# Kernel tuning notes

Measured on AMD Instinct MI355X. Metric: run time of the kernel, lower is better.

The kernel has to match this reference:

```python
import jax, jax.numpy as jnp
import numpy as np

B, T, C = 4, 2048, 1024
H, D = 16, 64


def setup_inputs() -> dict:
    key = jax.random.key(0)
    ks = jax.random.split(key, 5)
    x = jax.random.normal(ks[0], (B, T, C), dtype=jnp.float32)
    Wq = jax.random.normal(ks[1], (H, C, D), dtype=jnp.float32) * (C ** -0.5)
    Wk = jax.random.normal(ks[2], (H, C, D), dtype=jnp.float32) * (C ** -0.5)
    Wv = jax.random.normal(ks[3], (H, C, D), dtype=jnp.float32) * (C ** -0.5)
    Wp = jax.random.normal(ks[4], (H * D, C), dtype=jnp.float32) * ((H * D) ** -0.5)
    bp = jnp.zeros((C,), dtype=jnp.float32)
    return {"x": x, "Wq": Wq, "Wk": Wk, "Wv": Wv, "Wp": Wp, "bp": bp}


def reference(x, Wq, Wk, Wv, Wp, bp):
    # per-head projections (bias-free): [B,H,T,D]
    q = jnp.einsum('btc,hcd->bhtd', x, Wq)
    k = jnp.einsum('btc,hcd->bhtd', x, Wk)
    v = jnp.einsum('btc,hcd->bhtd', x, Wv)
    # NOTE: source multiplies by sqrt(head_size) (faithful to original code)
    scale = jnp.asarray(D ** 0.5, x.dtype)
    att = jnp.einsum('bhtd,bhsd->bhts', q, k) * scale  # [B,H,T,T]
    causal = jnp.tril(jnp.ones((T, T), dtype=bool))
    att = jnp.where(causal, att, jnp.asarray(-jnp.inf, att.dtype))
    att = jax.nn.softmax(att, axis=-1)
    out = jnp.einsum('bhts,bhsd->bhtd', att, v)  # [B,H,T,D]
    out = out.transpose(0, 2, 1, 3).reshape(B, T, H * D)  # head concat
    return out @ Wp + bp
```

## Files before the change

kernel.cpp:

```cpp
#include <hip/hip_runtime.h>

#define B_ 4
#define T_ 2048
#define C_ 1024
#define H_ 16
#define D_ 64

typedef _Float16 f16x8 __attribute__((ext_vector_type(8)));
typedef __fp16 fp16x2 __attribute__((ext_vector_type(2)));
typedef float f32x4 __attribute__((ext_vector_type(4)));
typedef unsigned short u16x8 __attribute__((ext_vector_type(8)));

#define MFMA16 __builtin_amdgcn_mfma_f32_16x16x32_f16
#define SCALE2 11.541560327111707f

__device__ __forceinline__ unsigned pk2(float a, float b) {
    fp16x2 p = __builtin_amdgcn_cvt_pkrtz(a, b);
    return __builtin_bit_cast(unsigned, p);
}

__device__ __forceinline__ void gl_lds16(const _Float16* g, unsigned short* lds) {
    __builtin_amdgcn_global_load_lds(
        (const __attribute__((address_space(1))) unsigned int*)g,
        (__attribute__((address_space(3))) unsigned int*)lds, 16, 0, 0);
}

__global__ __launch_bounds__(256) void convx_kernel(const float* __restrict__ x,
                                                    _Float16* __restrict__ Xf) {
    size_t i = ((size_t)blockIdx.x * 256 + threadIdx.x) * 8;
    f32x4 a = *reinterpret_cast<const f32x4*>(x + i);
    f32x4 b = *reinterpret_cast<const f32x4*>(x + i + 4);
    f16x8 o;
    o[0] = (_Float16)a[0]; o[1] = (_Float16)a[1]; o[2] = (_Float16)a[2]; o[3] = (_Float16)a[3];
    o[4] = (_Float16)b[0]; o[5] = (_Float16)b[1]; o[6] = (_Float16)b[2]; o[7] = (_Float16)b[3];
    *reinterpret_cast<f16x8*>(Xf + i) = o;
}

__global__ __launch_bounds__(256) void convw_qkv_kernel(
    const float* __restrict__ Wq, const float* __restrict__ Wk, const float* __restrict__ Wv,
    _Float16* __restrict__ Wqt, _Float16* __restrict__ Wkt, _Float16* __restrict__ Wvt)
{
    __shared__ unsigned short Wl[128][72];
    const int ct = blockIdx.x, h = blockIdx.y, m = blockIdx.z;
    const float* src = (m == 0 ? Wq : (m == 1 ? Wk : Wv)) + ((size_t)h * C_ + ct * 128) * D_;
    _Float16* dst = (m == 0 ? Wqt : (m == 1 ? Wkt : Wvt));
    const int tid = threadIdx.x;
    {
        int r = tid >> 1, half = tid & 1;
        #pragma unroll
        for (int i = 0; i < 8; i++) {
            f32x4 v = *reinterpret_cast<const f32x4*>(src + (size_t)r * D_ + half * 32 + i * 4);
            #pragma unroll
            for (int j = 0; j < 4; j++)
                Wl[r][half * 32 + i * 4 + j] = __builtin_bit_cast(unsigned short, (_Float16)v[j]);
        }
    }
    __syncthreads();
    {
        int d = tid >> 2, seg = tid & 3;
        #pragma unroll
        for (int i = 0; i < 4; i++) {
            u16x8 o;
            #pragma unroll
            for (int j = 0; j < 8; j++) o[j] = Wl[seg * 32 + i * 8 + j][d];
            *reinterpret_cast<u16x8*>((unsigned short*)dst + ((size_t)h * D_ + d) * C_ + ct * 128 + seg * 32 + i * 8) = o;
        }
    }
}

__global__ __launch_bounds__(256) void convw_p_kernel(const float* __restrict__ Wp,
                                                      _Float16* __restrict__ Wpt)
{
    __shared__ unsigned short Pl[64][72];
    const int jt = blockIdx.x, kt = blockIdx.y;
    const int tid = threadIdx.x;
    {
        int r = tid >> 2, seg = tid & 3;
        #pragma unroll
        for (int i = 0; i < 4; i++) {
            f32x4 v = *reinterpret_cast<const f32x4*>(Wp + (size_t)(kt * 64 + r) * C_ + jt * 64 + seg * 16 + i * 4);
            #pragma unroll
            for (int j = 0; j < 4; j++)
                Pl[r][seg * 16 + i * 4 + j] = __builtin_bit_cast(unsigned short, (_Float16)v[j]);
        }
    }
    __syncthreads();
    {
        int jj = tid >> 2, kseg = tid & 3;
        #pragma unroll
        for (int i = 0; i < 2; i++) {
            u16x8 o;
            #pragma unroll
            for (int j = 0; j < 8; j++) o[j] = Pl[kseg * 16 + i * 8 + j][jj];
            *reinterpret_cast<u16x8*>((unsigned short*)Wpt + (size_t)(jt * 64 + jj) * C_ + kt * 64 + kseg * 16 + i * 8) = o;
        }
    }
}

__global__ __launch_bounds__(256) void qkv4_kernel(
    const _Float16* __restrict__ Xf, const _Float16* __restrict__ Wcat,
    _Float16* __restrict__ Qf, _Float16* __restrict__ Kf, _Float16* __restrict__ Vt)
{
    __shared__ unsigned short As[128 * 64];
    __shared__ unsigned short Bs[192 * 64];
    const int rt = blockIdx.x, ct = blockIdx.y;
    const int row0 = rt * 128, n0 = ct * 192;
    const int tid = threadIdx.x, wid = tid >> 6, lane = tid & 63;
    const int l15 = lane & 15, g = lane >> 4;
    const int wr = wid >> 1, wc = wid & 1;
    const int lrow = lane >> 3, lcol = (lane & 7) * 8;

    f32x4 acc[4][6];
    #pragma unroll
    for (int mi = 0; mi < 4; mi++)
        #pragma unroll
        for (int ni = 0; ni < 6; ni++) { f32x4 z = {0.f,0.f,0.f,0.f}; acc[mi][ni] = z; }

    for (int k0 = 0; k0 < C_; k0 += 64) {
        __syncthreads();
        #pragma unroll
        for (int i = 0; i < 4; i++) {
            int c = wid * 4 + i;
            gl_lds16(Xf + (size_t)(row0 + c * 8 + lrow) * C_ + k0 + lcol, &As[c * 512]);
        }
        #pragma unroll
        for (int i = 0; i < 6; i++) {
            int c = wid * 6 + i;
            gl_lds16(Wcat + (size_t)(n0 + c * 8 + lrow) * C_ + k0 + lcol, &Bs[c * 512]);
        }
        __syncthreads();
        #pragma unroll
        for (int kk = 0; kk < 2; kk++) {
            f16x8 af[4];
            #pragma unroll
            for (int mi = 0; mi < 4; mi++)
                af[mi] = *reinterpret_cast<const f16x8*>(&As[(wr * 64 + mi * 16 + l15) * 64 + kk * 32 + g * 8]);
            #pragma unroll
            for (int ni = 0; ni < 6; ni++) {
                f16x8 bf = *reinterpret_cast<const f16x8*>(&Bs[(wc * 96 + ni * 16 + l15) * 64 + kk * 32 + g * 8]);
                #pragma unroll
                for (int mi = 0; mi < 4; mi++)
                    acc[mi][ni] = MFMA16(af[mi], bf, acc[mi][ni], 0, 0, 0);
            }
        }
    }

    const int b = row0 >> 11;
    const int t0b = (row0 & (T_ - 1)) + wr * 64;
    #pragma unroll
    for (int ni = 0; ni < 6; ni++) {
        const int n = n0 + wc * 96 + ni * 16;
        const int region = n >> 10;
        const int h = (n >> 6) & 15;
        const int d0 = n & 63;
        if (region < 2) {
            _Float16* dst = region ? Kf : Qf;
            const float osc = region ? 1.0f : SCALE2;
            const size_t hb = ((size_t)(b * H_ + h)) * T_ * D_;
            #pragma unroll
            for (int mi = 0; mi < 4; mi++)
                #pragma unroll
                for (int r = 0; r < 4; r++) {
                    int t = t0b + mi * 16 + g * 4 + r;
                    dst[hb + (size_t)t * D_ + d0 + l15] = (_Float16)(acc[mi][ni][r] * osc);
                }
        } else {
            const size_t vbase = ((size_t)(b * H_ + h)) * D_ * T_;
            const int d = d0 + l15;
            #pragma unroll
            for (int mi = 0; mi < 4; mi++) {
                int t = t0b + mi * 16 + g * 4;
                uint2 w;
                w.x = pk2(acc[mi][ni][0], acc[mi][ni][1]);
                w.y = pk2(acc[mi][ni][2], acc[mi][ni][3]);
                *reinterpret_cast<uint2*>((unsigned short*)Vt + vbase + (size_t)d * T_ + t) = w;
            }
        }
    }
}

__global__ __launch_bounds__(256) void flash_kernel(
    const _Float16* __restrict__ Qf, const _Float16* __restrict__ Kf,
    const _Float16* __restrict__ Vt, _Float16* __restrict__ att)
{
    __shared__ __align__(16) unsigned short Ks[2][64 * 64];
    __shared__ __align__(16) unsigned short Vs[2][64 * 64];
    __shared__ __align__(16) unsigned short Ps[4][32 * 32];
    const int bh = blockIdx.x;
    const int p = (int)blockIdx.y;
    const int bb = bh >> 4, h = bh & 15;
    const int tid = threadIdx.x, wid = tid >> 6, lane = tid & 63;
    const int l15 = lane & 15, g = lane >> 4;

    const _Float16* Qb = Qf + (size_t)bh * T_ * D_;
    const _Float16* Kb = Kf + (size_t)bh * T_ * D_;
    const _Float16* Vb = Vt + (size_t)bh * D_ * T_;

    const int srow = lane >> 3;
    const int sunit = (lane & 7) ^ srow;
    const int r0s = wid * 16;

    char* const pbase = (char*)&Ps[wid][0];

    for (int pass = 0; pass < 2; pass++) {
        const int qt = pass ? p : (15 - p);
        const int q0 = qt * 128;
        const int qw = q0 + wid * 32;

        f16x8 qf[2][2];
        #pragma unroll
        for (int mt = 0; mt < 2; mt++)
            #pragma unroll
            for (int kk = 0; kk < 2; kk++)
                qf[mt][kk] = *reinterpret_cast<const f16x8*>(Qb + (size_t)(qw + mt * 16 + l15) * D_ + kk * 32 + g * 8);

        f32x4 accO[4][2];
        #pragma unroll
        for (int nt = 0; nt < 4; nt++)
            #pragma unroll
            for (int mt = 0; mt < 2; mt++) { f32x4 z = {0.f,0.f,0.f,0.f}; accO[nt][mt] = z; }
        float m[2] = { -1e30f, -1e30f };
        float l[2] = { 0.f, 0.f };

        const int myNt = (qw + 95) >> 6;
        const int ntB  = (q0 + 191) >> 6;

        #pragma unroll
        for (int i = 0; i < 2; i++) {
            int row = r0s + i * 8 + srow;
            gl_lds16(Kb + (size_t)row * D_ + sunit * 8, &Ks[0][(r0s + i * 8) * 64]);
            gl_lds16(Vb + (size_t)row * T_ + sunit * 8, &Vs[0][(r0s + i * 8) * 64]);
        }
        __syncthreads();

#define TILE_BODY(TI, BUF)                                                          \
    {                                                                               \
        const int kv0 = (TI) * 64;                                                  \
        if ((TI) + 1 < ntB) {                                                       \
            const int kvn = kv0 + 64;                                               \
            _Pragma("unroll")                                                       \
            for (int i = 0; i < 2; i++) {                                           \
                int row = r0s + i * 8 + srow;                                       \
                gl_lds16(Kb + (size_t)(kvn + row) * D_ + sunit * 8,                 \
                         &Ks[(BUF) ^ 1][(r0s + i * 8) * 64]);                       \
                gl_lds16(Vb + (size_t)row * T_ + kvn + sunit * 8,                   \
                         &Vs[(BUF) ^ 1][(r0s + i * 8) * 64]);                       \
            }                                                                       \
        }                                                                           \
        if ((TI) < myNt) {                                                          \
            const bool maskt = ((TI) == myNt - 1);                                  \
            const char* kbase = (const char*)&Ks[BUF][0];                           \
            const char* vbase = (const char*)&Vs[BUF][0];                           \
            f32x4 s[4][2];                                                          \
            _Pragma("unroll")                                                       \
            for (int st = 0; st < 4; st++)                                          \
                _Pragma("unroll")                                                   \
                for (int mt = 0; mt < 2; mt++) { f32x4 z = {0.f,0.f,0.f,0.f}; s[st][mt] = z; } \
            _Pragma("unroll")                                                       \
            for (int kk = 0; kk < 2; kk++) {                                        \
                f16x8 kfr[4];                                                       \
                _Pragma("unroll")                                                   \
                for (int st = 0; st < 4; st++) {                                    \
                    int row = st * 16 + l15;                                        \
                    kfr[st] = *reinterpret_cast<const f16x8*>(                      \
                        kbase + row * 128 + (((kk * 4 + g) ^ (row & 7)) * 16));     \
                }                                                                   \
                _Pragma("unroll")                                                   \
                for (int st = 0; st < 4; st++)                                      \
                    _Pragma("unroll")                                               \
                    for (int mt = 0; mt < 2; mt++)                                  \
                        s[st][mt] = MFMA16(kfr[st], qf[mt][kk], s[st][mt], 0, 0, 0);\
            }                                                                       \
            unsigned pw[2][4][2];                                                   \
            _Pragma("unroll")                                                       \
            for (int mt = 0; mt < 2; mt++) {                                        \
                const int r = mt * 16 + l15;                                        \
                const int qrow = qw + r;                                            \
                float lv[4][4];                                                     \
                float vmax = -1e30f;                                                \
                _Pragma("unroll")                                                   \
                for (int st = 0; st < 4; st++)                                      \
                    _Pragma("unroll")                                               \
                    for (int rr = 0; rr < 4; rr++) {                                \
                        float v = s[st][mt][rr];                                    \
                        if (maskt) {                                                \
                            int kv = kv0 + st * 16 + g * 4 + rr;                    \
                            v = (kv <= qrow) ? v : -1e30f;                          \
                        }                                                           \
                        lv[st][rr] = v;                                             \
                        vmax = fmaxf(vmax, v);                                      \
                    }                                                               \
                vmax = fmaxf(vmax, __shfl_xor(vmax, 16, 64));                       \
                vmax = fmaxf(vmax, __shfl_xor(vmax, 32, 64));                       \
                float mnew = fmaxf(m[mt], vmax);                                    \
                float alpha = __builtin_amdgcn_exp2f(m[mt] - mnew);                 \
                m[mt] = mnew;                                                       \
                float rs = 0.f;                                                     \
                _Pragma("unroll")                                                   \
                for (int st = 0; st < 4; st++) {                                    \
                    float p0 = __builtin_amdgcn_exp2f(lv[st][0] - mnew);            \
                    float p1 = __builtin_amdgcn_exp2f(lv[st][1] - mnew);            \
                    float p2 = __builtin_amdgcn_exp2f(lv[st][2] - mnew);            \
                    float p3 = __builtin_amdgcn_exp2f(lv[st][3] - mnew);            \
                    rs += (p0 + p1) + (p2 + p3);                                    \
                    pw[mt][st][0] = pk2(p0, p1);                                    \
                    pw[mt][st][1] = pk2(p2, p3);                                    \
                }                                                                   \
                rs += __shfl_xor(rs, 16, 64);                                       \
                rs += __shfl_xor(rs, 32, 64);                                       \
                l[mt] = l[mt] * alpha + rs;                                         \
                _Pragma("unroll")                                                   \
                for (int nt = 0; nt < 4; nt++) accO[nt][mt] *= alpha;               \
            }                                                                       \
            _Pragma("unroll")                                                       \
            for (int half = 0; half < 2; half++) {                                  \
                _Pragma("unroll")                                                   \
                for (int mt = 0; mt < 2; mt++) {                                    \
                    const int r = mt * 16 + l15;                                    \
                    const int swz = ((r >> 1) & 3) << 4;                            \
                    char* prow = pbase + r * 64;                                    \
                    _Pragma("unroll")                                               \
                    for (int stl = 0; stl < 2; stl++) {                             \
                        uint2 w;                                                    \
                        w.x = pw[mt][half * 2 + stl][0];                            \
                        w.y = pw[mt][half * 2 + stl][1];                            \
                        *reinterpret_cast<uint2*>(prow + ((stl * 32 + g * 8) ^ swz)) = w; \
                    }                                                               \
                }                                                                   \
                f16x8 pb[2];                                                        \
                _Pragma("unroll")                                                   \
                for (int mt = 0; mt < 2; mt++) {                                    \
                    const int r = mt * 16 + l15;                                    \
                    const int swz = ((r >> 1) & 3) << 4;                            \
                    pb[mt] = *reinterpret_cast<const f16x8*>(pbase + r * 64 + ((g * 16) ^ swz)); \
                }                                                                   \
                _Pragma("unroll")                                                   \
                for (int nt = 0; nt < 4; nt++) {                                    \
                    int row = nt * 16 + l15;                                        \
                    f16x8 vf = *reinterpret_cast<const f16x8*>(                     \
                        vbase + row * 128 + (((half * 4 + g) ^ (row & 7)) * 16));   \
                    _Pragma("unroll")                                               \
                    for (int mt = 0; mt < 2; mt++)                                  \
                        accO[nt][mt] = MFMA16(vf, pb[mt], accO[nt][mt], 0, 0, 0);   \
                }                                                                   \
            }                                                                       \
        }                                                                           \
        __syncthreads();                                                            \
    }

        for (int tI = 0; tI < ntB; tI += 2) {
            TILE_BODY(tI, 0)
            if (tI + 1 < ntB) {
                TILE_BODY(tI + 1, 1)
            }
        }
#undef TILE_BODY

        #pragma unroll
        for (int mt = 0; mt < 2; mt++) {
            float inv = 1.0f / l[mt];
            int t = qw + mt * 16 + l15;
            #pragma unroll
            for (int nt = 0; nt < 4; nt++) {
                f32x4 o = accO[nt][mt] * inv;
                uint2 w;
                w.x = pk2(o[0], o[1]);
                w.y = pk2(o[2], o[3]);
                size_t off = ((size_t)(bb * T_ + t)) * (H_ * D_) + h * D_ + nt * 16 + g * 4;
                *reinterpret_cast<uint2*>((unsigned short*)att + off) = w;
            }
        }
    }
}

__global__ __launch_bounds__(256) void proj2_kernel(
    const _Float16* __restrict__ att, const _Float16* __restrict__ Wpt,
    const float* __restrict__ bp, float* __restrict__ out)
{
    __shared__ unsigned short As[128 * 64];
    __shared__ unsigned short Bs[128 * 64];
    const int rt = blockIdx.x, ct = blockIdx.y;
    const int row0 = rt * 128, n0 = ct * 128;
    const int tid = threadIdx.x, wid = tid >> 6, lane = tid & 63;
    const int l15 = lane & 15, g = lane >> 4;
    const int wr = wid >> 1, wc = wid & 1;
    const int lrow = lane >> 3, lcol = (lane & 7) * 8;

    f32x4 acc[4][4];
    #pragma unroll
    for (int mi = 0; mi < 4; mi++)
        #pragma unroll
        for (int ni = 0; ni < 4; ni++) { f32x4 z = {0.f,0.f,0.f,0.f}; acc[mi][ni] = z; }

    for (int k0 = 0; k0 < C_; k0 += 64) {
        __syncthreads();
        #pragma unroll
        for (int i = 0; i < 4; i++) {
            int c = wid * 4 + i;
            gl_lds16(att + (size_t)(row0 + c * 8 + lrow) * C_ + k0 + lcol, &As[c * 512]);
            gl_lds16(Wpt + (size_t)(n0   + c * 8 + lrow) * C_ + k0 + lcol, &Bs[c * 512]);
        }
        __syncthreads();
        #pragma unroll
        for (int kk = 0; kk < 2; kk++) {
            f16x8 af[4], bf[4];
            #pragma unroll
            for (int mi = 0; mi < 4; mi++)
                af[mi] = *reinterpret_cast<const f16x8*>(&As[(wr * 64 + mi * 16 + l15) * 64 + kk * 32 + g * 8]);
            #pragma unroll
            for (int ni = 0; ni < 4; ni++)
                bf[ni] = *reinterpret_cast<const f16x8*>(&Bs[(wc * 64 + ni * 16 + l15) * 64 + kk * 32 + g * 8]);
            #pragma unroll
            for (int mi = 0; mi < 4; mi++)
                #pragma unroll
                for (int ni = 0; ni < 4; ni++)
                    acc[mi][ni] = MFMA16(af[mi], bf[ni], acc[mi][ni], 0, 0, 0);
        }
    }

    #pragma unroll
    for (int mi = 0; mi < 4; mi++)
        #pragma unroll
        for (int ni = 0; ni < 4; ni++) {
            int col = n0 + wc * 64 + ni * 16 + l15;
            float bias = bp[col];
            #pragma unroll
            for (int r = 0; r < 4; r++) {
                int row = row0 + wr * 64 + mi * 16 + g * 4 + r;
                out[(size_t)row * C_ + col] = acc[mi][ni][r] + bias;
            }
        }
}

extern "C" void kernel_launch(void* const* d_in, const int* in_sizes, int n_in,
                              void* d_out, int out_size, void* d_ws, size_t ws_size,
                              hipStream_t stream) {
    const float* x  = (const float*)d_in[0];
    const float* Wq = (const float*)d_in[1];
    const float* Wk = (const float*)d_in[2];
    const float* Wv = (const float*)d_in[3];
    const float* Wp = (const float*)d_in[4];
    const float* bp = (const float*)d_in[5];
    float* out = (float*)d_out;

    _Float16* Xf  = (_Float16*)d_ws;
    _Float16* Wqt = Xf  + (size_t)8388608;
    _Float16* Wkt = Wqt + (size_t)1048576;
    _Float16* Wvt = Wkt + (size_t)1048576;
    _Float16* Wpt = Wvt + (size_t)1048576;
    _Float16* Qf  = Wpt + (size_t)1048576;
    _Float16* Kf  = Qf  + (size_t)8388608;
    _Float16* Vt  = Kf  + (size_t)8388608;
    _Float16* att = Vt  + (size_t)8388608;

    convx_kernel<<<4096, 256, 0, stream>>>(x, Xf);
    convw_qkv_kernel<<<dim3(8, 16, 3), 256, 0, stream>>>(Wq, Wk, Wv, Wqt, Wkt, Wvt);
    convw_p_kernel<<<dim3(16, 16), 256, 0, stream>>>(Wp, Wpt);
    qkv4_kernel<<<dim3(64, 16), 256, 0, stream>>>(Xf, Wqt, Qf, Kf, Vt);
    flash_kernel<<<dim3(64, 8), 256, 0, stream>>>(Qf, Kf, Vt, att);
    proj2_kernel<<<dim3(64, 8), 256, 0, stream>>>(att, Wpt, bp, out);
}
```

Measured before the change: 195.5 us.

## Stage 128-row KV super-tiles in LDS and skip rescale when max unchanged

The flash attention kernel now loads K and V into LDS in 128-key super-tiles, double-buffered, and runs two 64-key sub-tiles per super-tile. This halves the number of block-wide barriers and prefetch rounds per query tile. It also adds a wave-uniform check that skips the accumulator and row-sum rescale when no row max increased. The cost is double the LDS footprint, which may reduce occupancy, and some extra masked work on the diagonal super-tile.

```diff
diff --git a/kernel.cpp b/kernel.cpp
--- a/kernel.cpp
+++ b/kernel.cpp
@@ -183,8 +183,8 @@
     const _Float16* __restrict__ Qf, const _Float16* __restrict__ Kf,
     const _Float16* __restrict__ Vt, _Float16* __restrict__ att)
 {
-    __shared__ __align__(16) unsigned short Ks[2][64 * 64];
-    __shared__ __align__(16) unsigned short Vs[2][64 * 64];
+    __shared__ __align__(16) unsigned short Ks[2][128 * 64];
+    __shared__ __align__(16) unsigned short Vs[2][64 * 128];
     __shared__ __align__(16) unsigned short Ps[4][32 * 32];
     const int bh = blockIdx.x;
     const int p = (int)blockIdx.y;
@@ -198,7 +198,9 @@
 
     const int srow = lane >> 3;
     const int sunit = (lane & 7) ^ srow;
-    const int r0s = wid * 16;
+    const int r0k = wid * 32;
+    const int vsrow = lane >> 4;
+    const int r0v = wid * 16;
 
     char* const pbase = (char*)&Ps[wid][0];
 
@@ -222,139 +224,150 @@
         float m[2] = { -1e30f, -1e30f };
         float l[2] = { 0.f, 0.f };
 
-        const int myNt = (qw + 95) >> 6;
-        const int ntB  = (q0 + 191) >> 6;
-
-        #pragma unroll
-        for (int i = 0; i < 2; i++) {
-            int row = r0s + i * 8 + srow;
-            gl_lds16(Kb + (size_t)row * D_ + sunit * 8, &Ks[0][(r0s + i * 8) * 64]);
-            gl_lds16(Vb + (size_t)row * T_ + sunit * 8, &Vs[0][(r0s + i * 8) * 64]);
+        const int nSup = qt + 1;
+        const int mySub = (qw + 95) >> 6;
+
+        #pragma unroll
+        for (int i = 0; i < 4; i++) {
+            int krow = r0k + i * 8 + srow;
+            gl_lds16(Kb + (size_t)krow * D_ + sunit * 8, &Ks[0][(r0k + i * 8) * 64]);
+            int vrow = r0v + i * 4 + vsrow;
+            int vsunit = (lane & 15) ^ (vrow & 7);
+            gl_lds16(Vb + (size_t)vrow * T_ + vsunit * 8, &Vs[0][(r0v + i * 4) * 128]);
         }
         __syncthreads();
 
-#define TILE_BODY(TI, BUF)                                                          \
+#define SUPER_BODY(SP, BUF)                                                         \
     {                                                                               \
-        const int kv0 = (TI) * 64;                                                  \
-        if ((TI) + 1 < ntB) {                                                       \
-            const int kvn = kv0 + 64;                                               \
+        if ((SP) + 1 < nSup) {                                                      \
+            const int kvn = ((SP) + 1) * 128;                                       \
             _Pragma("unroll")                                                       \
-            for (int i = 0; i < 2; i++) {                                           \
-                int row = r0s + i * 8 + srow;                                       \
-                gl_lds16(Kb + (size_t)(kvn + row) * D_ + sunit * 8,                 \
-                         &Ks[(BUF) ^ 1][(r0s + i * 8) * 64]);                       \
-                gl_lds16(Vb + (size_t)row * T_ + kvn + sunit * 8,                   \
-                         &Vs[(BUF) ^ 1][(r0s + i * 8) * 64]);                       \
+            for (int i = 0; i < 4; i++) {                                           \
+                int krow = r0k + i * 8 + srow;                                      \
+                gl_lds16(Kb + (size_t)(kvn + krow) * D_ + sunit * 8,                \
+                         &Ks[(BUF) ^ 1][(r0k + i * 8) * 64]);                       \
+                int vrow = r0v + i * 4 + vsrow;                                     \
+                int vsunit = (lane & 15) ^ (vrow & 7);                              \
+                gl_lds16(Vb + (size_t)vrow * T_ + kvn + vsunit * 8,                 \
+                         &Vs[(BUF) ^ 1][(r0v + i * 4) * 128]);                      \
             }                                                                       \
         }                                                                           \
-        if ((TI) < myNt) {                                                          \
-            const bool maskt = ((TI) == myNt - 1);                                  \
-            const char* kbase = (const char*)&Ks[BUF][0];                           \
-            const char* vbase = (const char*)&Vs[BUF][0];                           \
-            f32x4 s[4][2];                                                          \
-            _Pragma("unroll")                                                       \
-            for (int st = 0; st < 4; st++)                                          \
+        const char* kb128 = (const char*)&Ks[BUF][0];                               \
+        const char* vb128 = (const char*)&Vs[BUF][0];                               \
+        _Pragma("unroll")                                                           \
+        for (int sh = 0; sh < 2; sh++) {                                            \
+            const int sI = (SP) * 2 + sh;                                           \
+            if (sI < mySub) {                                                       \
+                const int kv0 = sI * 64;                                            \
+                const bool maskt = (sI == mySub - 1);                               \
+                f32x4 s[4][2];                                                      \
                 _Pragma("unroll")                                                   \
-                for (int mt = 0; mt < 2; mt++) { f32x4 z = {0.f,0.f,0.f,0.f}; s[st][mt] = z; } \
-            _Pragma("unroll")                                                       \
-            for (int kk = 0; kk < 2; kk++) {                                        \
-                f16x8 kfr[4];                                                       \
+                for (int st = 0; st < 4; st++)                                      \
+                    _Pragma("unroll")                                               \
+                    for (int mt = 0; mt < 2; mt++) { f32x4 z = {0.f,0.f,0.f,0.f}; s[st][mt] = z; } \
                 _Pragma("unroll")                                                   \
-                for (int st = 0; st < 4; st++) {                                    \
-                    int row = st * 16 + l15;                                        \
-                    kfr[st] = *reinterpret_cast<const f16x8*>(                      \
-                        kbase + row * 128 + (((kk * 4 + g) ^ (row & 7)) * 16));     \
+                for (int kk = 0; kk < 2; kk++) {                                    \
+                    f16x8 kfr[4];                                                   \
+                    _Pragma("unroll")                                               \
+                    for (int st = 0; st < 4; st++) {                                \
+                        int row = sh * 64 + st * 16 + l15;                          \
+                        kfr[st] = *reinterpret_cast<const f16x8*>(                  \
+                            kb128 + row * 128 + (((kk * 4 + g) ^ (row & 7)) * 16)); \
+                    }                                                               \
+                    _Pragma("unroll")                                               \
+                    for (int st = 0; st < 4; st++)                                  \
+                        _Pragma("unroll")                                           \
+                        for (int mt = 0; mt < 2; mt++)                              \
+                            s[st][mt] = MFMA16(kfr[st], qf[mt][kk], s[st][mt], 0, 0, 0); \
+                }                                                                   \
+                unsigned pw[2][4][2];                                               \
+                _Pragma("unroll")                                                   \
+                for (int mt = 0; mt < 2; mt++) {                                    \
+                    const int qrow = qw + mt * 16 + l15;                            \
+                    float lv[4][4];                                                 \
+                    float vmax = -1e30f;                                            \
+                    _Pragma("unroll")                                               \
+                    for (int st = 0; st < 4; st++)                                  \
+                        _Pragma("unroll")                                           \
+                        for (int rr = 0; rr < 4; rr++) {                            \
+                            float v = s[st][mt][rr];                                \
+                            if (maskt) {                                            \
+                                int kv = kv0 + st * 16 + g * 4 + rr;                \
+                                v = (kv <= qrow) ? v : -1e30f;                      \
+                            }                                                       \
+                            lv[st][rr] = v;                                         \
+                            vmax = fmaxf(vmax, v);                                  \
+                        }                                                           \
+                    vmax = fmaxf(vmax, __shfl_xor(vmax, 16, 64));                   \
+                    vmax = fmaxf(vmax, __shfl_xor(vmax, 32, 64));                   \
+                    if (__any(vmax > m[mt])) {                                      \
+                        float mnew = fmaxf(m[mt], vmax);                            \
+                        float alpha = __builtin_amdgcn_exp2f(m[mt] - mnew);         \
+                        m[mt] = mnew;                                               \
+                        l[mt] *= alpha;                                             \
+                        _Pragma("unroll")                                           \
+                        for (int nt = 0; nt < 4; nt++) accO[nt][mt] *= alpha;       \
+                    }                                                               \
+                    float rs = 0.f;                                                 \
+                    _Pragma("unroll")                                               \
+                    for (int st = 0; st < 4; st++) {                                \
+                        float p0 = __builtin_amdgcn_exp2f(lv[st][0] - m[mt]);       \
+                        float p1 = __builtin_amdgcn_exp2f(lv[st][1] - m[mt]);       \
+                        float p2 = __builtin_amdgcn_exp2f(lv[st][2] - m[mt]);       \
+                        float p3 = __builtin_amdgcn_exp2f(lv[st][3] - m[mt]);       \
+                        rs += (p0 + p1) + (p2 + p3);                                \
+                        pw[mt][st][0] = pk2(p0, p1);                                \
+                        pw[mt][st][1] = pk2(p2, p3);                                \
+                    }                                                               \
+                    rs += __shfl_xor(rs, 16, 64);                                   \
+                    rs += __shfl_xor(rs, 32, 64);                                   \
+                    l[mt] += rs;                                                    \
                 }                                                                   \
                 _Pragma("unroll")                                                   \
-                for (int st = 0; st < 4; st++)                                      \
-                    _Pragma("unroll")                                               \
-                    for (int mt = 0; mt < 2; mt++)                                  \
-                        s[st][mt] = MFMA16(kfr[st], qf[mt][kk], s[st][mt], 0, 0, 0);\
-            }                                                                       \
-            unsigned pw[2][4][2];                                                   \
-            _Pragma("unroll")                                                       \
-            for (int mt = 0; mt < 2; mt++) {                                        \
-                const int r = mt * 16 + l15;                                        \
-                const int qrow = qw + r;                                            \
-                float lv[4][4];                                                     \
-                float vmax = -1e30f;                                                \
-                _Pragma("unroll")                                                   \
-                for (int st = 0; st < 4; st++)                                      \
-                    _Pragma("unroll")                                               \
-                    for (int rr = 0; rr < 4; rr++) {                                \
-                        float v = s[st][mt][rr];                                    \
-                        if (maskt) {                                                \
-                            int kv = kv0 + st * 16 + g * 4 + rr;                    \
-                            v = (kv <= qrow) ? v : -1e30f;                          \
+                for (int ph = 0; ph < 2; ph++) {                                    \
+                    _Pragma("unroll")                                               \
+                    for (int mt = 0; mt < 2; mt++) {                                \
+                        const int r = mt * 16 + l15;                                \
+                        const int swz = ((r >> 1) & 3) << 4;                        \
+                        char* prow = pbase + r * 64;                                \
+                        _Pragma("unroll")                                           \
+                        for (int stl = 0; stl < 2; stl++) {                         \
+                            uint2 w;                                                \
+                            w.x = pw[mt][ph * 2 + stl][0];                          \
+                            w.y = pw[mt][ph * 2 + stl][1];                          \
+                            *reinterpret_cast<uint2*>(prow + ((stl * 32 + g * 8) ^ swz)) = w; \
                         }                                                           \
-                        lv[st][rr] = v;                                             \
-                        vmax = fmaxf(vmax, v);                                      \
-                    }                                                               \
-                vmax = fmaxf(vmax, __shfl_xor(vmax, 16, 64));                       \
-                vmax = fmaxf(vmax, __shfl_xor(vmax, 32, 64));                       \
-                float mnew = fmaxf(m[mt], vmax);                                    \
-                float alpha = __builtin_amdgcn_exp2f(m[mt] - mnew);                 \
-                m[mt] = mnew;                                                       \
-                float rs = 0.f;                                                     \
-                _Pragma("unroll")                                                   \
-                for (int st = 0; st < 4; st++) {                                    \
-                    float p0 = __builtin_amdgcn_exp2f(lv[st][0] - mnew);            \
-                    float p1 = __builtin_amdgcn_exp2f(lv[st][1] - mnew);            \
-                    float p2 = __builtin_amdgcn_exp2f(lv[st][2] - mnew);            \
-                    float p3 = __builtin_amdgcn_exp2f(lv[st][3] - mnew);            \
-                    rs += (p0 + p1) + (p2 + p3);                                    \
-                    pw[mt][st][0] = pk2(p0, p1);                                    \
-                    pw[mt][st][1] = pk2(p2, p3);                                    \
-                }                                                                   \
-                rs += __shfl_xor(rs, 16, 64);                                       \
-                rs += __shfl_xor(rs, 32, 64);                                       \
-                l[mt] = l[mt] * alpha + rs;                                         \
-                _Pragma("unroll")                                                   \
-                for (int nt = 0; nt < 4; nt++) accO[nt][mt] *= alpha;               \
-            }                                                                       \
-            _Pragma("unroll")                                                       \
-            for (int half = 0; half < 2; half++) {                                  \
-                _Pragma("unroll")                                                   \
-                for (int mt = 0; mt < 2; mt++) {                                    \
-                    const int r = mt * 16 + l15;                                    \
-                    const int swz = ((r >> 1) & 3) << 4;                            \
-                    char* prow = pbase + r * 64;                                    \
-                    _Pragma("unroll")                                               \
-                    for (int stl = 0; stl < 2; stl++) {                             \
-                        uint2 w;                                                    \
-                        w.x = pw[mt][half * 2 + stl][0];                            \
-                        w.y = pw[mt][half * 2 + stl][1];                            \
-                        *reinterpret_cast<uint2*>(prow + ((stl * 32 + g * 8) ^ swz)) = w; \
-                    }                                                               \
-                }                                                                   \
-                f16x8 pb[2];                                                        \
-                _Pragma("unroll")                                                   \
-                for (int mt = 0; mt < 2; mt++) {                                    \
-                    const int r = mt * 16 + l15;                                    \
-                    const int swz = ((r >> 1) & 3) << 4;                            \
-                    pb[mt] = *reinterpret_cast<const f16x8*>(pbase + r * 64 + ((g * 16) ^ swz)); \
-                }                                                                   \
-                _Pragma("unroll")                                                   \
-                for (int nt = 0; nt < 4; nt++) {                                    \
-                    int row = nt * 16 + l15;                                        \
-                    f16x8 vf = *reinterpret_cast<const f16x8*>(                     \
-                        vbase + row * 128 + (((half * 4 + g) ^ (row & 7)) * 16));   \
-                    _Pragma("unroll")                                               \
-                    for (int mt = 0; mt < 2; mt++)                                  \
-                        accO[nt][mt] = MFMA16(vf, pb[mt], accO[nt][mt], 0, 0, 0);   \
+                    }                                                               \
+                    f16x8 pb[2];                                                    \
+                    _Pragma("unroll")                                               \
+                    for (int mt = 0; mt < 2; mt++) {                                \
+                        const int r = mt * 16 + l15;                                \
+                        const int swz = ((r >> 1) & 3) << 4;                        \
+                        pb[mt] = *reinterpret_cast<const f16x8*>(pbase + r * 64 + ((g * 16) ^ swz)); \
+                    }                                                               \
+                    _Pragma("unroll")                                               \
+                    for (int nt = 0; nt < 4; nt++) {                                \
+                        int row = nt * 16 + l15;                                    \
+                        int unit = (sh * 8 + ph * 4 + g) ^ (row & 7);               \
+                        f16x8 vf = *reinterpret_cast<const f16x8*>(                 \
+                            vb128 + row * 256 + unit * 16);                         \
+                        _Pragma("unroll")                                           \
+                        for (int mt = 0; mt < 2; mt++)                              \
+                            accO[nt][mt] = MFMA16(vf, pb[mt], accO[nt][mt], 0, 0, 0); \
+                    }                                                               \
                 }                                                                   \
             }                                                                       \
         }                                                                           \
         __syncthreads();                                                            \
     }
 
-        for (int tI = 0; tI < ntB; tI += 2) {
-            TILE_BODY(tI, 0)
-            if (tI + 1 < ntB) {
-                TILE_BODY(tI + 1, 1)
+        for (int sp = 0; sp < nSup; sp += 2) {
+            SUPER_BODY(sp, 0)
+            if (sp + 1 < nSup) {
+                SUPER_BODY(sp + 1, 1)
             }
         }
-#undef TILE_BODY
+#undef SUPER_BODY
 
         #pragma unroll
         for (int mt = 0; mt < 2; mt++) {
```

After: 195.3 us. No clear change (-0.1%).
